# Kernel optimization log

Hardware: AMD Instinct MI355X
Metric: run time of the kernel (lower is better)

## Reference

```python
import jax, jax.numpy as jnp
import numpy as np

N, M, F_IN, F_OUT, B = 8192, 4096, 256, 128, 2048
NEG = -9e15
EPS = 1e-5


def leaky(x, slope=0.2):
    return jnp.where(x > 0, x, slope * x)


def batchnorm(x, gamma, beta):
    # BatchNorm1d training-mode semantics: biased batch stats over dim 0
    m = x.mean(axis=0)
    v = jnp.var(x, axis=0)
    return (x - m) * jax.lax.rsqrt(v + EPS) * gamma + beta


def setup_inputs() -> dict:
    key = jax.random.key(0)
    ks = jax.random.split(key, 12)
    inp = {}
    inp["Sinput"] = jax.random.normal(ks[0], (N, F_IN), dtype=jnp.float32)
    inp["Rinput"] = jax.random.normal(ks[1], (M, F_IN), dtype=jnp.float32)
    inp["inter_adj"] = jax.random.randint(ks[2], (N, M), 0, 2).astype(jnp.int32)
    inp["city_adj"] = jax.random.randint(ks[3], (N, N), 0, 2).astype(jnp.int32)
    inp["province_adj"] = jax.random.randint(ks[4], (N, N), 0, 2).astype(jnp.int32)
    inp["source_index"] = jax.random.randint(ks[5], (B,), 0, N).astype(jnp.int32)
    s_w = 1.414 * np.sqrt(6.0 / (F_IN + F_OUT))  # xavier_uniform gain=1.414
    s_a = 1.414 * np.sqrt(6.0 / (2 * F_OUT + 1))
    inp["W1"] = jax.random.uniform(ks[6], (F_IN, F_OUT), jnp.float32, -s_w, s_w)
    inp["W2"] = jax.random.uniform(ks[7], (F_IN, F_OUT), jnp.float32, -s_w, s_w)
    inp["a"] = jax.random.uniform(ks[8], (2 * F_OUT, 1), jnp.float32, -s_a, s_a)
    inp["a3"] = jax.random.uniform(ks[9], (2 * F_OUT, 1), jnp.float32, -s_a, s_a)
    inp["a4"] = jax.random.uniform(ks[10], (2 * F_OUT, 1), jnp.float32, -s_a, s_a)
    inp["bn1_gamma"] = jnp.ones((F_OUT,), jnp.float32)
    inp["bn1_beta"] = jnp.zeros((F_OUT,), jnp.float32)
    inp["bn2_gamma"] = jnp.ones((F_OUT,), jnp.float32)
    inp["bn2_beta"] = jnp.zeros((F_OUT,), jnp.float32)
    return inp


def reference(Sinput, Rinput, inter_adj, city_adj, province_adj, source_index,
              W1, W2, a, a3, a4, bn1_gamma, bn1_beta, bn2_gamma, bn2_beta):
    F = W1.shape[1]
    h1 = Rinput @ W1            # [M, F]
    h2 = Sinput @ W2            # [N, F]
    # Decomposed GAT score: cat([h1[m], h2[n]]) @ a == h1[m]@a[:F] + h2[n]@a[F:]
    e12 = leaky((h2 @ a[F:, 0])[:, None] + (h1 @ a[:F, 0])[None, :])  # [N, M]
    att_inter = jax.nn.softmax(jnp.where(inter_adj > 0, e12, NEG), axis=1)
    h2_ = h2[source_index]      # [B, F]
    # cat([h2_, h2_]) @ a3 -> h2_ @ (a3[:F] + a3[F:]), constant along N axis
    s3 = leaky(h2_ @ (a3[:F, 0] + a3[F:, 0]))  # [B]
    s4 = leaky(h2_ @ (a4[:F, 0] + a4[F:, 0]))  # [B]
    Nn = Sinput.shape[0]
    e3 = jnp.broadcast_to(s3[:, None], (s3.shape[0], Nn))
    e4 = jnp.broadcast_to(s4[:, None], (s4.shape[0], Nn))
    att3 = jax.nn.softmax(jnp.where(city_adj[source_index] > 0, e3, NEG), axis=1)
    att4 = jax.nn.softmax(jnp.where(province_adj[source_index] > 0, e4, NEG), axis=1)
    InterRC = att_inter @ h1                    # [N, F]
    IntraNC = att3.T @ h2_ + att4.T @ h2_       # [N, F]
    v_output = leaky(batchnorm(att_inter.T @ h2, bn1_gamma, bn1_beta))  # [M, F]
    u_output = leaky(batchnorm(InterRC + IntraNC, bn2_gamma, bn2_beta))  # [N, F]
    h_prime = u_output @ v_output.T             # [N, M]
    return jax.nn.elu(h_prime)
```

## Files before the change

### kernel.cpp

```cpp
#include <hip/hip_runtime.h>
#include <stdint.h>

#define N_ 8192
#define M_ 4096
#define FIN_ 256
#define F_ 128
#define B_ 2048

typedef __attribute__((ext_vector_type(8))) short vs8;
typedef __attribute__((ext_vector_type(8))) __bf16 vb8;
typedef __attribute__((ext_vector_type(4))) float vf4;

union ABu { vs8 s; vb8 b; };

__device__ __forceinline__ vf4 mfma16(const ABu& a, const ABu& b, vf4 c) {
    return __builtin_amdgcn_mfma_f32_16x16x32_bf16(a.b, b.b, c, 0, 0, 0);
}
__device__ __forceinline__ unsigned short f2b(float x) {
    union { float f; unsigned u; } v; v.f = x;
    unsigned r = v.u + 0x7fffu + ((v.u >> 16) & 1u);
    return (unsigned short)(r >> 16);
}
__device__ __forceinline__ float lrelu(float x) { return x > 0.f ? x : 0.2f * x; }

__global__ void k_prep(const float* __restrict__ W1, const float* __restrict__ W2,
                       unsigned short* __restrict__ W1T, unsigned short* __restrict__ W2T,
                       float4* __restrict__ Z, int nz4) {
    int id = blockIdx.x * 256 + threadIdx.x;
    if (id < 65536) {
        const float* W = (id < 32768) ? W1 : W2;
        unsigned short* WT = (id < 32768) ? W1T : W2T;
        int o = id & 32767;
        int f = o >> 8, k = o & 255;
        WT[o] = f2b(W[k * F_ + f]);
    } else {
        int z = id - 65536;
        if (z < nz4) Z[z] = make_float4(0.f, 0.f, 0.f, 0.f);
    }
}

__global__ __launch_bounds__(256) void k_hgemmF(const float* __restrict__ Rin, const float* __restrict__ Sin,
                                                const unsigned short* __restrict__ W1T,
                                                const unsigned short* __restrict__ W2T,
                                                const float* __restrict__ a,
                                                float* __restrict__ h2,
                                                unsigned short* __restrict__ h1P, unsigned short* __restrict__ h2P,
                                                float* __restrict__ s1, float* __restrict__ s2) {
    __shared__ unsigned short tb[16][136];
    __shared__ float sred[4][16];
    int t = threadIdx.x;
    int w = t >> 6, l = t & 63, lr = l & 15, lg = l >> 4;
    int gr = blockIdx.x * 16;
    const float* X; const unsigned short* WT; unsigned short* HP; float* sout; const float* av;
    int row0; bool isH2;
    if (gr < M_) { X = Rin; WT = W1T; HP = h1P; sout = s1; av = a;      row0 = gr;      isH2 = false; }
    else         { X = Sin; WT = W2T; HP = h2P; sout = s2; av = a + F_; row0 = gr - M_; isH2 = true;  }
    int fbase = w * 32;
    vf4 acc[2] = {};
    const float* xp = X + (size_t)(row0 + lr) * FIN_ + lg * 8;
#pragma unroll
    for (int kk = 0; kk < FIN_; kk += 32) {
        float4 xa = *(const float4*)(xp + kk);
        float4 xb = *(const float4*)(xp + kk + 4);
        ABu af;
        af.s[0] = (short)f2b(xa.x); af.s[1] = (short)f2b(xa.y);
        af.s[2] = (short)f2b(xa.z); af.s[3] = (short)f2b(xa.w);
        af.s[4] = (short)f2b(xb.x); af.s[5] = (short)f2b(xb.y);
        af.s[6] = (short)f2b(xb.z); af.s[7] = (short)f2b(xb.w);
#pragma unroll
        for (int q = 0; q < 2; ++q) {
            ABu bf; bf.s = *(const vs8*)(WT + (fbase + q * 16 + lr) * FIN_ + kk + lg * 8);
            acc[q] = mfma16(af, bf, acc[q]);
        }
    }
    if (isH2) {
#pragma unroll
        for (int q = 0; q < 2; ++q)
#pragma unroll
            for (int r = 0; r < 4; ++r)
                h2[(size_t)(row0 + lg * 4 + r) * F_ + fbase + q * 16 + lr] = acc[q][r];
    }
#pragma unroll
    for (int q = 0; q < 2; ++q)
#pragma unroll
        for (int r = 0; r < 4; ++r)
            tb[lg * 4 + r][fbase + q * 16 + lr] = f2b(acc[q][r]);
    float a0 = av[fbase + lr], a1 = av[fbase + 16 + lr];
    float tv[4];
#pragma unroll
    for (int r = 0; r < 4; ++r) tv[r] = acc[0][r] * a0 + acc[1][r] * a1;
#pragma unroll
    for (int off = 1; off < 16; off <<= 1)
#pragma unroll
        for (int r = 0; r < 4; ++r) tv[r] += __shfl_xor(tv[r], off, 64);
    if ((l & 15) == 0)
#pragma unroll
        for (int r = 0; r < 4; ++r) sred[w][lg * 4 + r] = tv[r];
    __syncthreads();
    {
        int f = t >> 1, half = t & 1;
        vs8 o;
#pragma unroll
        for (int j = 0; j < 8; ++j) o[j] = (short)tb[half * 8 + j][f];
        *(vs8*)(HP + ((size_t)(row0 >> 5) * 128 + f) * 32 + (row0 & 16) + half * 8) = o;
    }
    if (t < 16) {
        float s = sred[0][t] + sred[1][t] + sred[2][t] + sred[3][t];
        sout[row0 + t] = s;
    }
}

__global__ __launch_bounds__(256) void k_adjgather(const int* __restrict__ inter, const float* __restrict__ s1,
                                                   const float* __restrict__ s2, unsigned short* __restrict__ bm,
                                                   float* __restrict__ rowmax, float* __restrict__ rowinv,
                                                   const int* __restrict__ city, const int* __restrict__ prov,
                                                   const int* __restrict__ src,
                                                   uint32_t* __restrict__ BMtc, uint32_t* __restrict__ BMtp,
                                                   float* __restrict__ w3, float* __restrict__ w4,
                                                   const float* __restrict__ h2, unsigned short* __restrict__ h2wP) {
    __shared__ float wred[8];
    int t = threadIdx.x;
    int wv = t >> 6, ln = t & 63;
    if (blockIdx.x < N_) {
        int n = blockIdx.x;
        const int* rp = inter + (size_t)n * M_ + t * 16;
        float sv[16]; unsigned mask = 0;
#pragma unroll
        for (int c = 0; c < 4; ++c) {
            int4 v = *(const int4*)(rp + c * 4);
            if (v.x > 0) mask |= 1u << (c * 4 + 0);
            if (v.y > 0) mask |= 1u << (c * 4 + 1);
            if (v.z > 0) mask |= 1u << (c * 4 + 2);
            if (v.w > 0) mask |= 1u << (c * 4 + 3);
            float4 s = *(const float4*)(s1 + t * 16 + c * 4);
            sv[c * 4 + 0] = s.x; sv[c * 4 + 1] = s.y; sv[c * 4 + 2] = s.z; sv[c * 4 + 3] = s.w;
        }
        bm[(size_t)n * 256 + t] = (unsigned short)(mask & 0xffffu);
        float mx = -3.0e38f;
#pragma unroll
        for (int j = 0; j < 16; ++j) if (mask & (1u << j)) mx = fmaxf(mx, sv[j]);
        for (int off = 32; off > 0; off >>= 1) mx = fmaxf(mx, __shfl_down(mx, off, 64));
        if (ln == 0) wred[wv] = mx;
        __syncthreads();
        float s1mx = fmaxf(fmaxf(wred[0], wred[1]), fmaxf(wred[2], wred[3]));
        float s2n = s2[n];
        float rmx = lrelu(s2n + s1mx);
        float sum = 0.f;
#pragma unroll
        for (int j = 0; j < 16; ++j) if (mask & (1u << j)) sum += __expf(lrelu(s2n + sv[j]) - rmx);
        for (int off = 32; off > 0; off >>= 1) sum += __shfl_down(sum, off, 64);
        if (ln == 0) wred[4 + wv] = sum;
        __syncthreads();
        if (t == 0) {
            float tot = wred[4] + wred[5] + wred[6] + wred[7];
            bool any = s1mx > -2.9e38f;
            rowmax[n] = any ? rmx : 0.f;
            rowinv[n] = (any && tot > 0.f) ? 1.0f / tot : 0.f;
        }
    } else if (blockIdx.x < N_ + 2 * B_) {
        int bb = blockIdx.x - N_;
        int b = bb & (B_ - 1);
        bool isC = bb < B_;
        const int* adj = isC ? city : prov;
        uint32_t* BM = isC ? BMtc : BMtp;
        float* wout = isC ? w3 : w4;
        const int* rowp = adj + (size_t)src[b] * N_;
        int cnt = 0;
#pragma unroll 4
        for (int i = 0; i < N_ / 256; ++i) {
            int v = rowp[i * 256 + t];
            unsigned long long bal = __ballot(v > 0);
            cnt += (v > 0);
            if (ln == 0) {
                int widx = i * 8 + wv * 2;
                BM[(size_t)widx * B_ + b] = (uint32_t)bal;
                BM[(size_t)(widx + 1) * B_ + b] = (uint32_t)(bal >> 32);
            }
        }
        float fc = (float)cnt;
        for (int off = 32; off > 0; off >>= 1) fc += __shfl_down(fc, off, 64);
        if (ln == 0) wred[wv] = fc;
        __syncthreads();
        if (t == 0) {
            float tot = wred[0] + wred[1] + wred[2] + wred[3];
            wout[b] = tot > 0.f ? 1.0f / tot : 0.f;
        }
    } else {
        int bblk = blockIdx.x - (N_ + 2 * B_);
        int f = t & 127, halfb = t >> 7;
        vs8 o0, o1;
#pragma unroll
        for (int i = 0; i < 8; ++i) {
            int b0 = bblk * 32 + halfb * 16 + i;
            o0[i] = (short)f2b(h2[(size_t)src[b0] * F_ + f]);
            int b1 = b0 + 8;
            o1[i] = (short)f2b(h2[(size_t)src[b1] * F_ + f]);
        }
        unsigned short* dst = h2wP + ((size_t)bblk * 128 + f) * 32 + halfb * 16;
        *(vs8*)dst = o0;
        *(vs8*)(dst + 8) = o1;
    }
}

__global__ __launch_bounds__(256) void k_attmat2(const unsigned char* __restrict__ bm8,
                                                 const float* __restrict__ s1, const float* __restrict__ s2,
                                                 const float* __restrict__ rowmax, const float* __restrict__ rowinv,
                                                 unsigned short* __restrict__ attP,
                                                 unsigned short* __restrict__ attT) {
    __shared__ unsigned short tile[64][33];
    int bx = blockIdx.x;
    int mt = bx & 63, nt = bx >> 6;
    int nb = nt * 32, mb = mt * 64;
    int t = threadIdx.x;
    int nl = t & 31, mo = t >> 5;
    int n = nb + nl;
    int m = mb + mo * 8;
    unsigned bits = bm8[(size_t)n * 512 + (m >> 3)];
    float s2n = s2[n], rmx = rowmax[n], rin = rowinv[n];
    float4 sa = *(const float4*)(s1 + m);
    float4 sb = *(const float4*)(s1 + m + 4);
    float sv[8] = {sa.x, sa.y, sa.z, sa.w, sb.x, sb.y, sb.z, sb.w};
    vs8 o;
#pragma unroll
    for (int j = 0; j < 8; ++j) {
        float v = (bits & (1u << j)) ? __expf(lrelu(s2n + sv[j]) - rmx) * rin : 0.f;
        o[j] = (short)f2b(v);
        tile[mo * 8 + j][nl] = (unsigned short)o[j];
    }
    *(vs8*)(attP + ((size_t)(m >> 5) * N_ + n) * 32 + (m & 31)) = o;
    __syncthreads();
    int mr = t >> 2, sg = t & 3;
    vs8 ot;
#pragma unroll
    for (int j = 0; j < 8; ++j) ot[j] = (short)tile[mr][sg * 8 + j];
    *(vs8*)(attT + ((size_t)nt * M_ + mb + mr) * 32 + sg * 8) = ot;
}

__global__ __launch_bounds__(256) void k_gemmABC(const unsigned short* __restrict__ attP,
                                                 const unsigned short* __restrict__ attT,
                                                 const unsigned short* __restrict__ h1P,
                                                 const unsigned short* __restrict__ h2P,
                                                 const uint32_t* __restrict__ BMtc, const uint32_t* __restrict__ BMtp,
                                                 const float* __restrict__ w3, const float* __restrict__ w4,
                                                 const unsigned short* __restrict__ h2wP,
                                                 float* __restrict__ u_in, float* __restrict__ v_in) {
    int t = threadIdx.x;
    int w = t >> 6, l = t & 63;
    int lr = l & 15, lg = l >> 4;
    int bx = blockIdx.x;
    if (bx < 1024) {
        bool isA = bx < 512;
        int i = isA ? bx : bx - 512;
        int x, y, nsteps, kbase;
        const unsigned short* Asrc; const unsigned short* Bsrc; float* Out;
        if (isA) { x = i & 127; y = i >> 7; nsteps = 32; kbase = y * 32;
                   Asrc = attP; Bsrc = h1P; Out = u_in; }
        else     { x = i & 63;  y = i >> 6; nsteps = 32; kbase = y * 32;
                   Asrc = attT; Bsrc = h2P; Out = v_in; }
        int rb0 = x * 64 + (w & 1) * 32;
        int fb = (w >> 1) * 64;
        vf4 acc[2][4] = {};
        int rowsK = isA ? N_ : M_;
        size_t aoff = (size_t)(rb0 + lr) * 32 + lg * 8;
        const unsigned short* apm = Asrc + (size_t)kbase * rowsK * 32 + aoff;
        size_t astride = (size_t)rowsK * 32;
        ABu a0, a1;
        a0.s = *(const vs8*)apm;
        a1.s = *(const vs8*)(apm + 16 * 32);
        for (int it = 0; it < 32; ++it) {
            const unsigned short* hb = Bsrc + (size_t)(kbase + it) * 128 * 32;
            ABu b0, b1, b2, b3;
            b0.s = *(const vs8*)(hb + (size_t)(fb + lr) * 32 + lg * 8);
            b1.s = *(const vs8*)(hb + (size_t)(fb + 16 + lr) * 32 + lg * 8);
            b2.s = *(const vs8*)(hb + (size_t)(fb + 32 + lr) * 32 + lg * 8);
            b3.s = *(const vs8*)(hb + (size_t)(fb + 48 + lr) * 32 + lg * 8);
            const unsigned short* apn = apm + (it < 31 ? astride : 0);
            ABu a0n, a1n;
            a0n.s = *(const vs8*)apn;
            a1n.s = *(const vs8*)(apn + 16 * 32);
            acc[0][0] = mfma16(a0, b0, acc[0][0]);
            acc[1][0] = mfma16(a1, b0, acc[1][0]);
            acc[0][1] = mfma16(a0, b1, acc[0][1]);
            acc[1][1] = mfma16(a1, b1, acc[1][1]);
            acc[0][2] = mfma16(a0, b2, acc[0][2]);
            acc[1][2] = mfma16(a1, b2, acc[1][2]);
            acc[0][3] = mfma16(a0, b3, acc[0][3]);
            acc[1][3] = mfma16(a1, b3, acc[1][3]);
            a0 = a0n; a1 = a1n;
            apm = apn;
        }
#pragma unroll
        for (int s = 0; s < 2; ++s)
#pragma unroll
            for (int q = 0; q < 4; ++q)
#pragma unroll
                for (int r = 0; r < 4; ++r)
                    atomicAdd(&Out[(size_t)(rb0 + s * 16 + lg * 4 + r) * F_ + fb + q * 16 + lr], acc[s][q][r]);
    } else {
        int i = bx - 1024;
        int xc = i & 127, yc = i >> 7;
        int nb0 = xc * 64 + (w & 1) * 32;
        int fb = (w >> 1) * 64;
        int wi = nb0 >> 5;
        const uint32_t* bc = BMtc + (size_t)wi * B_;
        const uint32_t* bp = BMtp + (size_t)wi * B_;
        vf4 acc[2][4] = {};
        int b0s = yc * (B_ / 4);
        for (int b0 = b0s; b0 < b0s + B_ / 4; b0 += 32) {
            int bb = b0 + lg * 8;
            uint4 c0 = *(const uint4*)(bc + bb);
            uint4 c1 = *(const uint4*)(bc + bb + 4);
            uint4 p0 = *(const uint4*)(bp + bb);
            uint4 p1 = *(const uint4*)(bp + bb + 4);
            float4 wa = *(const float4*)(w3 + bb);
            float4 wb = *(const float4*)(w3 + bb + 4);
            float4 wc = *(const float4*)(w4 + bb);
            float4 wd = *(const float4*)(w4 + bb + 4);
            const unsigned short* hb = h2wP + (size_t)(b0 >> 5) * 128 * 32;
            ABu bf0, bf1, bf2, bf3;
            bf0.s = *(const vs8*)(hb + (size_t)(fb + lr) * 32 + lg * 8);
            bf1.s = *(const vs8*)(hb + (size_t)(fb + 16 + lr) * 32 + lg * 8);
            bf2.s = *(const vs8*)(hb + (size_t)(fb + 32 + lr) * 32 + lg * 8);
            bf3.s = *(const vs8*)(hb + (size_t)(fb + 48 + lr) * 32 + lg * 8);
            uint32_t cw[8] = {c0.x, c0.y, c0.z, c0.w, c1.x, c1.y, c1.z, c1.w};
            uint32_t pw[8] = {p0.x, p0.y, p0.z, p0.w, p1.x, p1.y, p1.z, p1.w};
            float w3v[8] = {wa.x, wa.y, wa.z, wa.w, wb.x, wb.y, wb.z, wb.w};
            float w4v[8] = {wc.x, wc.y, wc.z, wc.w, wd.x, wd.y, wd.z, wd.w};
            ABu af0, af1;
#pragma unroll
            for (int j = 0; j < 8; ++j) {
                float v0 = (((cw[j] >> lr) & 1u) ? w3v[j] : 0.f) + (((pw[j] >> lr) & 1u) ? w4v[j] : 0.f);
                float v1 = (((cw[j] >> (16 + lr)) & 1u) ? w3v[j] : 0.f) + (((pw[j] >> (16 + lr)) & 1u) ? w4v[j] : 0.f);
                af0.s[j] = (short)f2b(v0);
                af1.s[j] = (short)f2b(v1);
            }
            acc[0][0] = mfma16(af0, bf0, acc[0][0]);
            acc[1][0] = mfma16(af1, bf0, acc[1][0]);
            acc[0][1] = mfma16(af0, bf1, acc[0][1]);
            acc[1][1] = mfma16(af1, bf1, acc[1][1]);
            acc[0][2] = mfma16(af0, bf2, acc[0][2]);
            acc[1][2] = mfma16(af1, bf2, acc[1][2]);
            acc[0][3] = mfma16(af0, bf3, acc[0][3]);
            acc[1][3] = mfma16(af1, bf3, acc[1][3]);
        }
#pragma unroll
        for (int s = 0; s < 2; ++s)
#pragma unroll
            for (int q = 0; q < 4; ++q)
#pragma unroll
                for (int r = 0; r < 4; ++r)
                    atomicAdd(&u_in[(size_t)(nb0 + s * 16 + lg * 4 + r) * F_ + fb + q * 16 + lr], acc[s][q][r]);
    }
}

__global__ __launch_bounds__(256) void k_bnstats2(const float* __restrict__ v_in, const float* __restrict__ u_in,
                                                  float* __restrict__ stats) {
    __shared__ float r1[256], r2[256];
    int bx = blockIdx.x;
    const float* P; int R, stride; float* sum; float* sq;
    if (bx < 256) { P = v_in; R = M_; stride = 512;  sum = stats;       sq = stats + 128; }
    else          { P = u_in; R = N_; stride = 1024; sum = stats + 256; sq = stats + 384; bx -= 256; }
    int f = threadIdx.x & 127;
    int half = threadIdx.x >> 7;
    float s = 0.f, s2v = 0.f;
    for (int r = bx * 2 + half; r < R; r += stride) {
        float v = P[(size_t)r * F_ + f];
        s += v; s2v += v * v;
    }
    r1[threadIdx.x] = s; r2[threadIdx.x] = s2v;
    __syncthreads();
    if (half == 0) {
        atomicAdd(&sum[f], r1[f] + r1[f + 128]);
        atomicAdd(&sq[f], r2[f] + r2[f + 128]);
    }
}

__global__ __launch_bounds__(256) void k_bnapplyF(const float* __restrict__ v_in, const float* __restrict__ u_in,
                                                  const float* __restrict__ stats,
                                                  const float* __restrict__ g1, const float* __restrict__ b1,
                                                  const float* __restrict__ g2, const float* __restrict__ b2,
                                                  unsigned short* __restrict__ v_outb, unsigned short* __restrict__ u_outb) {
    __shared__ float sc[256], sh[256];
    int t = threadIdx.x;
    {
        int which = t >> 7, f = t & 127;
        const float* sum = stats + which * 256;
        const float* sq = sum + 128;
        const float* g = which ? g2 : g1;
        const float* be = which ? b2 : b1;
        float R = which ? (float)N_ : (float)M_;
        float mean = sum[f] / R;
        float var = sq[f] / R - mean * mean;
        float s = g[f] * rsqrtf(var + 1e-5f);
        sc[t] = s; sh[t] = be[f] - mean * s;
    }
    __syncthreads();
    int id4 = blockIdx.x * 256 + t;
    int idx = id4 * 4;
    int which = idx >= M_ * F_;
    int rel = which ? idx - M_ * F_ : idx;
    const float* P = which ? u_in : v_in;
    unsigned short* Q = which ? u_outb : v_outb;
    int f0 = (rel & 127) + which * 128;
    float4 p = *(const float4*)(P + rel);
    ushort4 o;
    o.x = f2b(lrelu(p.x * sc[f0 + 0] + sh[f0 + 0]));
    o.y = f2b(lrelu(p.y * sc[f0 + 1] + sh[f0 + 1]));
    o.z = f2b(lrelu(p.z * sc[f0 + 2] + sh[f0 + 2]));
    o.w = f2b(lrelu(p.w * sc[f0 + 3] + sh[f0 + 3]));
    *(ushort4*)(Q + rel) = o;
}

__global__ __launch_bounds__(256) void k_gemmD(const unsigned short* __restrict__ U,
                                               const unsigned short* __restrict__ V,
                                               float* __restrict__ out) {
    int w = threadIdx.x >> 6, l = threadIdx.x & 63;
    int lr = l & 15, lg = l >> 4;
    int nb = blockIdx.x * 64 + w * 16;
    int mb = blockIdx.y * 64;
    vf4 acc[4] = {};
#pragma unroll
    for (int k0 = 0; k0 < F_; k0 += 32) {
        ABu af; af.s = *(const vs8*)(U + (size_t)(nb + lr) * F_ + k0 + lg * 8);
#pragma unroll
        for (int q = 0; q < 4; ++q) {
            ABu bf; bf.s = *(const vs8*)(V + (size_t)(mb + q * 16 + lr) * F_ + k0 + lg * 8);
            acc[q] = mfma16(af, bf, acc[q]);
        }
    }
#pragma unroll
    for (int q = 0; q < 4; ++q)
#pragma unroll
        for (int r = 0; r < 4; ++r) {
            int row = nb + lg * 4 + r;
            int col = mb + q * 16 + lr;
            float x = acc[q][r];
            out[(size_t)row * M_ + col] = x > 0.f ? x : __expf(x) - 1.f;
        }
}

extern "C" void kernel_launch(void* const* d_in, const int* in_sizes, int n_in,
                              void* d_out, int out_size, void* d_ws, size_t ws_size,
                              hipStream_t stream) {
    const float* Sinput = (const float*)d_in[0];
    const float* Rinput = (const float*)d_in[1];
    const int* inter_adj = (const int*)d_in[2];
    const int* city_adj = (const int*)d_in[3];
    const int* prov_adj = (const int*)d_in[4];
    const int* src = (const int*)d_in[5];
    const float* W1 = (const float*)d_in[6];
    const float* W2 = (const float*)d_in[7];
    const float* a = (const float*)d_in[8];
    const float* g1 = (const float*)d_in[11];
    const float* b1 = (const float*)d_in[12];
    const float* g2 = (const float*)d_in[13];
    const float* b2 = (const float*)d_in[14];
    float* out = (float*)d_out;

    char* ws = (char*)d_ws;
    size_t o = 0;
    auto take = [&](size_t bytes) { char* p = ws + o; o += (bytes + 255) & ~(size_t)255; return p; };
    float* u_in = (float*)take((size_t)N_ * F_ * 4);
    float* v_in = (float*)take((size_t)M_ * F_ * 4);
    float* stats = (float*)take(512 * 4);
    size_t zero_bytes = o;
    float* h2 = (float*)take((size_t)N_ * F_ * 4);
    unsigned short* h1P = (unsigned short*)take((size_t)(M_ / 32) * 128 * 32 * 2);
    unsigned short* h2P = (unsigned short*)take((size_t)(N_ / 32) * 128 * 32 * 2);
    unsigned short* W1T = (unsigned short*)take((size_t)F_ * FIN_ * 2);
    unsigned short* W2T = (unsigned short*)take((size_t)F_ * FIN_ * 2);
    float* s1 = (float*)take(M_ * 4);
    float* s2 = (float*)take(N_ * 4);
    float* rowmax = (float*)take(N_ * 4);
    float* rowinv = (float*)take(N_ * 4);
    float* w3 = (float*)take(B_ * 4);
    float* w4 = (float*)take(B_ * 4);
    unsigned short* h2wP = (unsigned short*)take((size_t)(B_ / 32) * 128 * 32 * 2);
    unsigned short* u_outb = (unsigned short*)take((size_t)N_ * F_ * 2);
    unsigned short* v_outb = (unsigned short*)take((size_t)M_ * F_ * 2);
    uint32_t* BMtc = (uint32_t*)take((size_t)256 * B_ * 4);
    uint32_t* BMtp = (uint32_t*)take((size_t)256 * B_ * 4);
    unsigned short* bm = (unsigned short*)take((size_t)N_ * 256 * 2);
    unsigned short* attP = (unsigned short*)take((size_t)N_ * M_ * 2);
    unsigned short* attT = (unsigned short*)take((size_t)N_ * M_ * 2);
    (void)ws_size; (void)in_sizes; (void)n_in; (void)out_size;

    int nz4 = (int)(zero_bytes / 16);
    int zblocks = (nz4 + 255) / 256;
    k_prep<<<256 + zblocks, 256, 0, stream>>>(W1, W2, W1T, W2T, (float4*)d_ws, nz4);
    k_hgemmF<<<(M_ + N_) / 16, 256, 0, stream>>>(Rinput, Sinput, W1T, W2T, a, h2, h1P, h2P, s1, s2);
    k_adjgather<<<N_ + 2 * B_ + B_ / 32, 256, 0, stream>>>(inter_adj, s1, s2, bm, rowmax, rowinv,
                                                           city_adj, prov_adj, src, BMtc, BMtp, w3, w4,
                                                           h2, h2wP);
    k_attmat2<<<16384, 256, 0, stream>>>((const unsigned char*)bm, s1, s2, rowmax, rowinv, attP, attT);
    k_gemmABC<<<1536, 256, 0, stream>>>(attP, attT, h1P, h2P, BMtc, BMtp, w3, w4, h2wP, u_in, v_in);
    k_bnstats2<<<768, 256, 0, stream>>>(v_in, u_in, stats);
    k_bnapplyF<<<(M_ + N_) * F_ / 4 / 256, 256, 0, stream>>>(v_in, u_in, stats, g1, b1, g2, b2, v_outb, u_outb);
    k_gemmD<<<dim3(N_ / 64, M_ / 64), 256, 0, stream>>>(u_outb, v_outb, out);
}
```

Before: 352.4 us.

## Replace split-K atomics with partial buffers reduced in BN stats kernel

The split-K GEMM blocks now write their partial tiles with plain stores into per-split slices (uP, vP) instead of issuing float atomicAdds into u_in and v_in. The BN statistics kernel is rewritten to sum the 8 partial slices, write the reduced u_in and v_in, and accumulate the stats in the same pass. Separately, the attention-matrix kernel swaps its thread index mapping so the m offset varies fastest, which changes the coalescing of the bitmask reads and the attP stores. This removes roughly 12M global atomics, but in exchange adds about 48 MB of partial-buffer writes plus the matching reads in the reduction kernel.

```diff
diff --git a/kernel.cpp b/kernel.cpp
--- a/kernel.cpp
+++ b/kernel.cpp
@@ -212,7 +212,7 @@
     int mt = bx & 63, nt = bx >> 6;
     int nb = nt * 32, mb = mt * 64;
     int t = threadIdx.x;
-    int nl = t & 31, mo = t >> 5;
+    int mo = t & 7, nl = t >> 3;
     int n = nb + nl;
     int m = mb + mo * 8;
     unsigned bits = bm8[(size_t)n * 512 + (m >> 3)];
@@ -243,7 +243,7 @@
                                                  const uint32_t* __restrict__ BMtc, const uint32_t* __restrict__ BMtp,
                                                  const float* __restrict__ w3, const float* __restrict__ w4,
                                                  const unsigned short* __restrict__ h2wP,
-                                                 float* __restrict__ u_in, float* __restrict__ v_in) {
+                                                 float* __restrict__ uP, float* __restrict__ vP) {
     int t = threadIdx.x;
     int w = t >> 6, l = t & 63;
     int lr = l & 15, lg = l >> 4;
@@ -251,12 +251,12 @@
     if (bx < 1024) {
         bool isA = bx < 512;
         int i = isA ? bx : bx - 512;
-        int x, y, nsteps, kbase;
+        int x, y, kbase;
         const unsigned short* Asrc; const unsigned short* Bsrc; float* Out;
-        if (isA) { x = i & 127; y = i >> 7; nsteps = 32; kbase = y * 32;
-                   Asrc = attP; Bsrc = h1P; Out = u_in; }
-        else     { x = i & 63;  y = i >> 6; nsteps = 32; kbase = y * 32;
-                   Asrc = attT; Bsrc = h2P; Out = v_in; }
+        if (isA) { x = i & 127; y = i >> 7; kbase = y * 32;
+                   Asrc = attP; Bsrc = h1P; Out = uP + (size_t)y * N_ * F_; }
+        else     { x = i & 63;  y = i >> 6; kbase = y * 32;
+                   Asrc = attT; Bsrc = h2P; Out = vP + (size_t)y * M_ * F_; }
         int rb0 = x * 64 + (w & 1) * 32;
         int fb = (w >> 1) * 64;
         vf4 acc[2][4] = {};
@@ -295,7 +295,7 @@
             for (int q = 0; q < 4; ++q)
 #pragma unroll
                 for (int r = 0; r < 4; ++r)
-                    atomicAdd(&Out[(size_t)(rb0 + s * 16 + lg * 4 + r) * F_ + fb + q * 16 + lr], acc[s][q][r]);
+                    Out[(size_t)(rb0 + s * 16 + lg * 4 + r) * F_ + fb + q * 16 + lr] = acc[s][q][r];
     } else {
         int i = bx - 1024;
         int xc = i & 127, yc = i >> 7;
@@ -343,28 +343,35 @@
             acc[0][3] = mfma16(af0, bf3, acc[0][3]);
             acc[1][3] = mfma16(af1, bf3, acc[1][3]);
         }
+        float* Out = uP + (size_t)(4 + yc) * N_ * F_;
 #pragma unroll
         for (int s = 0; s < 2; ++s)
 #pragma unroll
             for (int q = 0; q < 4; ++q)
 #pragma unroll
                 for (int r = 0; r < 4; ++r)
-                    atomicAdd(&u_in[(size_t)(nb0 + s * 16 + lg * 4 + r) * F_ + fb + q * 16 + lr], acc[s][q][r]);
-    }
-}
-
-__global__ __launch_bounds__(256) void k_bnstats2(const float* __restrict__ v_in, const float* __restrict__ u_in,
+                    Out[(size_t)(nb0 + s * 16 + lg * 4 + r) * F_ + fb + q * 16 + lr] = acc[s][q][r];
+    }
+}
+
+__global__ __launch_bounds__(256) void k_bnreduce(const float* __restrict__ vP, const float* __restrict__ uP,
+                                                  float* __restrict__ v_in, float* __restrict__ u_in,
                                                   float* __restrict__ stats) {
     __shared__ float r1[256], r2[256];
     int bx = blockIdx.x;
-    const float* P; int R, stride; float* sum; float* sq;
-    if (bx < 256) { P = v_in; R = M_; stride = 512;  sum = stats;       sq = stats + 128; }
-    else          { P = u_in; R = N_; stride = 1024; sum = stats + 256; sq = stats + 384; bx -= 256; }
+    const float* P; float* O; int R, nb_; size_t stride; float* sum; float* sq;
+    if (bx < 256) { P = vP; O = v_in; R = M_; nb_ = 256; stride = (size_t)M_ * F_;
+                    sum = stats; sq = stats + 128; }
+    else          { P = uP; O = u_in; R = N_; nb_ = 512; stride = (size_t)N_ * F_;
+                    sum = stats + 256; sq = stats + 384; bx -= 256; }
     int f = threadIdx.x & 127;
     int half = threadIdx.x >> 7;
     float s = 0.f, s2v = 0.f;
-    for (int r = bx * 2 + half; r < R; r += stride) {
-        float v = P[(size_t)r * F_ + f];
+    for (int r = bx * 2 + half; r < R; r += nb_ * 2) {
+        float v = 0.f;
+#pragma unroll
+        for (int y = 0; y < 8; ++y) v += P[(size_t)y * stride + (size_t)r * F_ + f];
+        O[(size_t)r * F_ + f] = v;
         s += v; s2v += v * v;
     }
     r1[threadIdx.x] = s; r2[threadIdx.x] = s2v;
@@ -460,10 +467,12 @@
     char* ws = (char*)d_ws;
     size_t o = 0;
     auto take = [&](size_t bytes) { char* p = ws + o; o += (bytes + 255) & ~(size_t)255; return p; };
+    float* stats = (float*)take(512 * 4);
+    size_t zero_bytes = o;
     float* u_in = (float*)take((size_t)N_ * F_ * 4);
     float* v_in = (float*)take((size_t)M_ * F_ * 4);
-    float* stats = (float*)take(512 * 4);
-    size_t zero_bytes = o;
+    float* uP = (float*)take((size_t)8 * N_ * F_ * 4);
+    float* vP = (float*)take((size_t)8 * M_ * F_ * 4);
     float* h2 = (float*)take((size_t)N_ * F_ * 4);
     unsigned short* h1P = (unsigned short*)take((size_t)(M_ / 32) * 128 * 32 * 2);
     unsigned short* h2P = (unsigned short*)take((size_t)(N_ / 32) * 128 * 32 * 2);
@@ -493,8 +502,8 @@
                                                            city_adj, prov_adj, src, BMtc, BMtp, w3, w4,
                                                            h2, h2wP);
     k_attmat2<<<16384, 256, 0, stream>>>((const unsigned char*)bm, s1, s2, rowmax, rowinv, attP, attT);
-    k_gemmABC<<<1536, 256, 0, stream>>>(attP, attT, h1P, h2P, BMtc, BMtp, w3, w4, h2wP, u_in, v_in);
-    k_bnstats2<<<768, 256, 0, stream>>>(v_in, u_in, stats);
+    k_gemmABC<<<1536, 256, 0, stream>>>(attP, attT, h1P, h2P, BMtc, BMtp, w3, w4, h2wP, uP, vP);
+    k_bnreduce<<<768, 256, 0, stream>>>(vP, uP, v_in, u_in, stats);
     k_bnapplyF<<<(M_ + N_) * F_ / 4 / 256, 256, 0, stream>>>(v_in, u_in, stats, g1, b1, g2, b2, v_outb, u_outb);
     k_gemmD<<<dim3(N_ / 64, M_ / 64), 256, 0, stream>>>(u_outb, v_outb, out);
 }
```

After: 347.8 us. No clear change (-1.3%).
